# Kernel optimization log

Measured on AMD Instinct MI355X. Metric: run time of the kernel, lower is better.

The kernel has to match this reference:

```python
import jax, jax.numpy as jnp
import numpy as np

# Mistral-7B layer-0 config
D, DKV, DFF, NH, NKV, HD, BLK, VOCAB = 4096, 1024, 14336, 32, 8, 128, 64, 32000
THETA = 10000.0
NF4_CODE = jnp.array([-1.0, -0.6961928009986877, -0.5250730514526367, -0.39491748809814453,
                      -0.28444138169288635, -0.18477343022823334, -0.09105003625154495, 0.0,
                      0.07958029955625534, 0.16093020141124725, 0.24611230194568634,
                      0.33791524171829224, 0.44070982933044434, 0.5626170039176941,
                      0.7229568362236023, 1.0], dtype=jnp.float32)


def dequant_nf4(idx, absmax):
    # idx: int [out,in] 4-bit codes; absmax: [numel/BLK] blockwise scales
    w = jnp.take(NF4_CODE, idx.reshape(-1, BLK)) * absmax[:, None]
    return w.reshape(idx.shape)


def rmsnorm(x, w, eps=1e-5):
    return x * jax.lax.rsqrt(jnp.mean(x * x, axis=-1, keepdims=True) + eps) * w


def rope(x, pos):
    # x: [B,S,H,HD] -- HF rotate-half convention
    half = HD // 2
    inv = 1.0 / (THETA ** (jnp.arange(0, half, dtype=jnp.float32) / half))
    f = pos[:, None] * inv[None, :]                      # [S, half]
    cos = jnp.concatenate([jnp.cos(f), jnp.cos(f)], -1)[None, :, None, :]
    sin = jnp.concatenate([jnp.sin(f), jnp.sin(f)], -1)[None, :, None, :]
    x1, x2 = x[..., :half], x[..., half:]
    rot = jnp.concatenate([-x2, x1], -1)
    return x * cos + rot * sin


def setup_inputs() -> dict:
    key = jax.random.key(0)
    ks = jax.random.split(key, 20)
    B, S = 4, 512
    inp = {}
    inp["input_ids"] = jax.random.randint(ks[0], (B, S), 0, VOCAB, dtype=jnp.int32)
    inp["attention_mask"] = jnp.ones((B, S), dtype=jnp.int32)
    inp["embed_table"] = jax.random.normal(ks[1], (VOCAB, D), dtype=jnp.float32) * 0.02
    shapes = {"q": (D, D), "k": (DKV, D), "v": (DKV, D), "o": (D, D),
              "gate": (DFF, D), "up": (DFF, D), "down": (D, DFF)}
    for i, (n, sh) in enumerate(shapes.items()):
        inp["idx_" + n] = jax.random.randint(ks[2 + i], sh, 0, 16, dtype=jnp.int32)
        inp["absmax_" + n] = jax.random.uniform(ks[9 + i], (sh[0] * sh[1] // BLK,), dtype=jnp.float32) * 0.02
    inp["rms1_w"] = jnp.ones((D,), jnp.float32)
    inp["rms2_w"] = jnp.ones((D,), jnp.float32)
    inp["dp_w"] = jax.random.normal(ks[16], (50, D), jnp.float32) * 0.02
    inp["dp_b"] = jnp.zeros((50,), jnp.float32)
    return inp


def reference(input_ids, attention_mask, embed_table,
              idx_q, idx_k, idx_v, idx_o, idx_gate, idx_up, idx_down,
              absmax_q, absmax_k, absmax_v, absmax_o, absmax_gate, absmax_up, absmax_down,
              rms1_w, rms2_w, dp_w, dp_b):
    B, S = input_ids.shape
    h = embed_table[input_ids]                            # [B,S,D]

    # --- Mistral decoder layer 0 (hidden_states[1]) ---
    r = rmsnorm(h, rms1_w)
    Wq = dequant_nf4(idx_q, absmax_q)
    Wk = dequant_nf4(idx_k, absmax_k)
    Wv = dequant_nf4(idx_v, absmax_v)
    Wo = dequant_nf4(idx_o, absmax_o)
    q = (r @ Wq.T).reshape(B, S, NH, HD)
    k = (r @ Wk.T).reshape(B, S, NKV, HD)
    v = (r @ Wv.T).reshape(B, S, NKV, HD)
    pos = jnp.arange(S, dtype=jnp.float32)
    q, k = rope(q, pos), rope(k, pos)
    rep = NH // NKV
    k = jnp.repeat(k, rep, axis=2)
    v = jnp.repeat(v, rep, axis=2)
    scores = jnp.einsum('bqhd,bkhd->bhqk', q, k) / np.float32(np.sqrt(HD))
    causal = jnp.tril(jnp.ones((S, S), bool))
    m = causal[None, None] & (attention_mask[:, None, None, :] > 0)
    scores = jnp.where(m, scores, jnp.float32(-1e9))
    p = jax.nn.softmax(scores, axis=-1)
    ao = jnp.einsum('bhqk,bkhd->bqhd', p, v).reshape(B, S, D)
    h = h + ao @ Wo.T

    r2 = rmsnorm(h, rms2_w)
    Wg = dequant_nf4(idx_gate, absmax_gate)
    Wu = dequant_nf4(idx_up, absmax_up)
    Wd = dequant_nf4(idx_down, absmax_down)
    h = h + (jax.nn.silu(r2 @ Wg.T) * (r2 @ Wu.T)) @ Wd.T

    # --- last_token_pool + L2 normalize ---
    last = jnp.sum(attention_mask, axis=-1) - 1           # [B]
    pooled = h[jnp.arange(B), last]                       # [B,D]
    pooled = pooled / jnp.maximum(jnp.linalg.norm(pooled, axis=1, keepdims=True), 1e-12)

    # --- down_projection + query*entity node embeddings ---
    emb = pooled @ dp_w.T + dp_b                          # [B,50]
    bs = B // 2
    node = emb[:bs] * emb[bs:]                            # [bs,50]
    return node
```

## Files before the change

### kernel.cpp

```cpp
#include <hip/hip_runtime.h>
#include <stdint.h>
#include <math.h>

#define TOK 2048
#define DMODEL 4096
#define DFF 14336
#define SEQ 512

typedef float f32x4 __attribute__((ext_vector_type(4)));
typedef short s16x8 __attribute__((ext_vector_type(8)));
typedef unsigned short u16x8 __attribute__((ext_vector_type(8)));

__constant__ float NF4_TAB[16] = {
  -1.0f, -0.6961928009986877f, -0.5250730514526367f, -0.39491748809814453f,
  -0.28444138169288635f, -0.18477343022823334f, -0.09105003625154495f, 0.0f,
  0.07958029955625534f, 0.16093020141124725f, 0.24611230194568634f,
  0.33791524171829224f, 0.44070982933044434f, 0.5626170039176941f,
  0.7229568362236023f, 1.0f };

__device__ __forceinline__ uint16_t f2bf(float f) {
  union { float f; uint32_t u; } x; x.f = f;
  uint32_t r = (x.u + 0x7FFFu + ((x.u >> 16) & 1u)) >> 16;
  return (uint16_t)r;
}
__device__ __forceinline__ float bf2f(uint16_t u) {
  union { uint32_t u; float f; } x; x.u = ((uint32_t)u) << 16;
  return x.f;
}
__device__ __forceinline__ f32x4 mfma16(s16x8 a, s16x8 b, f32x4 c) {
  return __builtin_amdgcn_mfma_f32_16x16x32_bf16(a, b, c, 0, 0, 0);
}
__device__ __forceinline__ void gload_lds16(const void* g, void* l) {
  __builtin_amdgcn_global_load_lds(
    (const __attribute__((address_space(1))) unsigned int*)g,
    (__attribute__((address_space(3))) unsigned int*)l, 16, 0, 0);
}

__global__ __launch_bounds__(256) void k_last(const int* __restrict__ maskp,
                                              int* __restrict__ lastb)
{
  int wv = threadIdx.x >> 6, l = threadIdx.x & 63;
  int cnt = 0;
  for (int j = l; j < SEQ; j += 64) cnt += (maskp[wv * SEQ + j] > 0);
  #pragma unroll
  for (int off = 1; off < 64; off <<= 1) cnt += __shfl_xor(cnt, off);
  if (l == 0) lastb[wv] = cnt - 1;
}

__global__ __launch_bounds__(256) void k_dequant(const int* __restrict__ idx,
    const float* __restrict__ am, uint16_t* __restrict__ out, int nelems, int K)
{
  __shared__ float code[16];
  if (threadIdx.x < 16) code[threadIdx.x] = NF4_TAB[threadIdx.x];
  __syncthreads();
  int nch = nelems >> 3;
  int stride = gridDim.x * 256;
  for (int c = blockIdx.x * 256 + threadIdx.x; c < nch; c += stride) {
    int e = c << 3;
    int row = e / K;
    int kc = e - row * K;
    float a = am[c >> 3];
    int4 i0 = *(const int4*)(idx + e);
    int4 i1 = *(const int4*)(idx + e + 4);
    u16x8 pk;
    pk[0] = f2bf(code[i0.x] * a);
    pk[1] = f2bf(code[i0.y] * a);
    pk[2] = f2bf(code[i0.z] * a);
    pk[3] = f2bf(code[i0.w] * a);
    pk[4] = f2bf(code[i1.x] * a);
    pk[5] = f2bf(code[i1.y] * a);
    pk[6] = f2bf(code[i1.z] * a);
    pk[7] = f2bf(code[i1.w] * a);
    int dk = (kc & ~63) | (((((kc >> 3) & 7) ^ (row & 7))) << 3);
    *(u16x8*)(out + (size_t)row * K + dk) = pk;
  }
}

__global__ __launch_bounds__(256) void k_rms(const int* __restrict__ ids,
    const float* __restrict__ table, const float* __restrict__ w,
    uint16_t* __restrict__ r)
{
  int t = blockIdx.x, tid = threadIdx.x;
  int wv = tid >> 6, l = tid & 63;
  const float* src = table + (size_t)ids[t] * DMODEL;
  int d0 = tid * 16;
  float vals[16];
  float ss = 0.f;
  #pragma unroll
  for (int i = 0; i < 4; ++i) {
    float4 v4 = *(const float4*)(src + d0 + i * 4);
    vals[i*4+0] = v4.x; vals[i*4+1] = v4.y; vals[i*4+2] = v4.z; vals[i*4+3] = v4.w;
    ss += v4.x*v4.x + v4.y*v4.y + v4.z*v4.z + v4.w*v4.w;
  }
  #pragma unroll
  for (int off = 1; off < 64; off <<= 1) ss += __shfl_xor(ss, off);
  __shared__ float red[4];
  if (l == 0) red[wv] = ss;
  __syncthreads();
  float rs = rsqrtf((red[0]+red[1]+red[2]+red[3]) * (1.f/DMODEL) + 1e-5f);
  #pragma unroll
  for (int cth = 0; cth < 2; ++cth) {
    int dd = d0 + cth * 8;
    u16x8 pk;
    #pragma unroll
    for (int j = 0; j < 8; ++j) pk[j] = f2bf(vals[cth*8+j] * rs * w[dd + j]);
    int dsw = (dd & ~63) | (((((dd >> 3) & 7) ^ (t & 7))) << 3);
    *(u16x8*)(r + (size_t)t * DMODEL + dsw) = pk;
  }
}

__global__ __launch_bounds__(512, 2) void k_gemmkv(
    const uint16_t* __restrict__ A, const uint16_t* __restrict__ W,
    float* __restrict__ pout)
{
  constexpr int K = 4096;
  constexpr int NT = 16;
  __shared__ __align__(1024) uint16_t As_[2 * 256 * 64];
  __shared__ __align__(1024) uint16_t Bs_[2 * 256 * 64];
  const int tid = threadIdx.x;
  const int wid = tid >> 6, l = tid & 63;
  const int wr = wid >> 2, wc = wid & 3;
  const int n0 = blockIdx.x * 256, m0 = blockIdx.y * 256;
  const size_t kbase = blockIdx.z * 1024;
  const int lrow = l >> 3, lcb = (l & 7) * 16;

  auto stA = [&](int t, int h) {
    int ta = (t < NT) ? t : (t - NT);
    const char* g = (const char*)A +
        ((size_t)(m0 + h * 128 + wid * 16 + lrow) * K + kbase + ta * 64) * 2 + lcb;
    char* s = (char*)As_ + (t & 1) * 32768 + h * 16384 + wid * 2048;
    gload_lds16(g, s);
    gload_lds16(g + (size_t)8 * K * 2, s + 1024);
  };
  auto stB = [&](int t, int h) {
    int ta = (t < NT) ? t : (t - NT);
    const char* g = (const char*)W +
        ((size_t)(n0 + h * 128 + wid * 16 + lrow) * K + kbase + ta * 64) * 2 + lcb;
    char* s = (char*)Bs_ + (t & 1) * 32768 + h * 16384 + wid * 2048;
    gload_lds16(g, s);
    gload_lds16(g + (size_t)8 * K * 2, s + 1024);
  };

  const int cb0 = (((l >> 4) << 4)) ^ ((l & 7) << 4);
  const int cb1 = (64 + ((l >> 4) << 4)) ^ ((l & 7) << 4);

  const f32x4 Z4 = {0.f, 0.f, 0.f, 0.f};
  f32x4 acc[8][4];
  #pragma unroll
  for (int i = 0; i < 8; ++i)
    #pragma unroll
    for (int j = 0; j < 4; ++j) acc[i][j] = Z4;
  s16x8 bfr[4][2];

#define VMW asm volatile("s_waitcnt vmcnt(6)" ::: "memory")
#define PHASE(DB, Q, READB, STG) {                                          \
    const char* abase = (const char*)As_ + (DB) * 32768;                    \
    s16x8 af[2][2];                                                         \
    _Pragma("unroll") for (int mm = 0; mm < 2; ++mm) {                      \
      int arow = ((2 * (2 * (Q) + mm) + wr) * 16 + (l & 15)) * 128;         \
      af[mm][0] = *(const s16x8*)(abase + arow + cb0);                      \
      af[mm][1] = *(const s16x8*)(abase + arow + cb1);                      \
    }                                                                       \
    if (READB) {                                                            \
      const char* bbase = (const char*)Bs_ + (DB) * 32768;                  \
      _Pragma("unroll") for (int nn = 0; nn < 4; ++nn) {                    \
        int brow = (wc * 64 + nn * 16 + (l & 15)) * 128;                    \
        bfr[nn][0] = *(const s16x8*)(bbase + brow + cb0);                   \
        bfr[nn][1] = *(const s16x8*)(bbase + brow + cb1);                   \
      }                                                                     \
    }                                                                       \
    STG;                                                                    \
    __builtin_amdgcn_s_barrier();                                           \
    asm volatile("s_waitcnt lgkmcnt(0)" ::: "memory");                      \
    __builtin_amdgcn_sched_barrier(0);                                      \
    __builtin_amdgcn_s_setprio(1);                                          \
    _Pragma("unroll") for (int mm = 0; mm < 2; ++mm)                        \
      _Pragma("unroll") for (int nn = 0; nn < 4; ++nn) {                    \
        acc[2 * (Q) + mm][nn] = mfma16(af[mm][0], bfr[nn][0], acc[2 * (Q) + mm][nn]); \
        acc[2 * (Q) + mm][nn] = mfma16(af[mm][1], bfr[nn][1], acc[2 * (Q) + mm][nn]); \
      }                                                                     \
    __builtin_amdgcn_s_setprio(0);                                          \
    __builtin_amdgcn_s_barrier();                                           \
  }

  stB(0, 0); stA(0, 0); stB(0, 1); stA(0, 1);
  stB(1, 0); stA(1, 0); stB(1, 1);
  VMW;
  __builtin_amdgcn_s_barrier();

  for (int it = 0; it < NT / 2; ++it) {
    int t0 = 2 * it, t1 = t0 + 1;
    PHASE(0, 0, 1, stA(t1, 1));
    PHASE(0, 1, 0, stB(t0 + 2, 0));
    PHASE(0, 2, 0, stA(t0 + 2, 0));
    PHASE(0, 3, 0, { stB(t0 + 2, 1); VMW; });
    PHASE(1, 0, 1, stA(t0 + 2, 1));
    PHASE(1, 1, 0, stB(t1 + 2, 0));
    PHASE(1, 2, 0, stA(t1 + 2, 0));
    PHASE(1, 3, 0, { stB(t1 + 2, 1); VMW; });
  }
  asm volatile("s_waitcnt vmcnt(0)" ::: "memory");
  __builtin_amdgcn_s_barrier();
#undef PHASE
#undef VMW

  float* po = pout + (size_t)blockIdx.z * 2048 * 2048;
  #pragma unroll
  for (int mf = 0; mf < 8; ++mf)
    #pragma unroll
    for (int nf = 0; nf < 4; ++nf)
      #pragma unroll
      for (int r = 0; r < 4; ++r) {
        int row = m0 + (2 * mf + wr) * 16 + ((l >> 4) << 2) + r;
        int col = n0 + wc * 64 + nf * 16 + (l & 15);
        po[(size_t)row * 2048 + col] = acc[mf][nf][r];
      }
}

__global__ __launch_bounds__(256) void k_redrope(const float* __restrict__ p,
    uint16_t* __restrict__ kv)
{
  int t = blockIdx.x, tid = threadIdx.x;
  const size_t zs = (size_t)2048 * 2048;
  auto sum4 = [&](int c) -> float {
    size_t o = (size_t)t * 2048 + c;
    return p[o] + p[o + zs] + p[o + 2 * zs] + p[o + 3 * zs];
  };
  float pos = (float)(t & (SEQ - 1));
  for (int pi = tid; pi < 512; pi += 256) {
    int hh = pi >> 6, j = pi & 63;
    int c1 = hh * 128 + j, c2 = c1 + 64;
    float s1 = sum4(c1), s2 = sum4(c2);
    float f = pos * expf(-(float)j * 0.14391156831212787f);
    float sn, cs;
    sincosf(f, &sn, &cs);
    kv[(size_t)t * 2048 + c1] = f2bf(s1 * cs - s2 * sn);
    kv[(size_t)t * 2048 + c2] = f2bf(s2 * cs + s1 * sn);
  }
  for (int c = 1024 + tid; c < 2048; c += 256)
    kv[(size_t)t * 2048 + c] = f2bf(sum4(c));
}

__global__ __launch_bounds__(256) void k_prep_r4(const uint16_t* __restrict__ rbuf,
    const int* __restrict__ lastb, float* __restrict__ r4f)
{
  int r = blockIdx.x;
  int t = r * SEQ + lastb[r];
  const uint16_t* src = rbuf + (size_t)t * DMODEL;
  for (int k = threadIdx.x * 8; k < DMODEL; k += 2048) {
    int so = (k & ~63) | (((((k >> 3) & 7) ^ (t & 7))) << 3);
    u16x8 v = *(const u16x8*)(src + so);
    #pragma unroll
    for (int j = 0; j < 8; ++j) r4f[r * DMODEL + k + j] = bf2f(v[j]);
  }
}

template<int MODE>
__global__ __launch_bounds__(256) void k_gemv4(const int* __restrict__ idx,
    const float* __restrict__ am, const float* __restrict__ a4,
    float* __restrict__ out, const float* __restrict__ table,
    const int* __restrict__ ids, const int* __restrict__ lastb)
{
  __shared__ float As[4 * 4096];
  __shared__ float code[16];
  if (threadIdx.x < 16) code[threadIdx.x] = NF4_TAB[threadIdx.x];
  for (int i = threadIdx.x * 4; i < 4 * 4096; i += 1024)
    *(float4*)(As + i) = *(const float4*)(a4 + i);
  __syncthreads();
  int wv = threadIdx.x >> 6, l = threadIdx.x & 63;
  int lhi = l >> 4;
  for (int n = blockIdx.x * 4 + wv; n < 4096; n += gridDim.x * 4) {
    const int4* ip = (const int4*)(idx + (size_t)n * 4096);
    const float* ap = am + (size_t)n * 64;
    float a0 = 0.f, a1 = 0.f, a2 = 0.f, a3 = 0.f;
    #pragma unroll
    for (int kk = 0; kk < 16; ++kk) {
      int4 iv = ip[kk * 64 + l];
      float sc = ap[kk * 4 + lhi];
      float w0 = code[iv.x] * sc, w1 = code[iv.y] * sc;
      float w2 = code[iv.z] * sc, w3 = code[iv.w] * sc;
      const float* A0 = As + kk * 256 + l * 4;
      f32x4 v0 = *(const f32x4*)A0;
      f32x4 v1 = *(const f32x4*)(A0 + 4096);
      f32x4 v2 = *(const f32x4*)(A0 + 8192);
      f32x4 v3 = *(const f32x4*)(A0 + 12288);
      a0 = fmaf(w0, v0[0], fmaf(w1, v0[1], fmaf(w2, v0[2], fmaf(w3, v0[3], a0))));
      a1 = fmaf(w0, v1[0], fmaf(w1, v1[1], fmaf(w2, v1[2], fmaf(w3, v1[3], a1))));
      a2 = fmaf(w0, v2[0], fmaf(w1, v2[1], fmaf(w2, v2[2], fmaf(w3, v2[3], a2))));
      a3 = fmaf(w0, v3[0], fmaf(w1, v3[1], fmaf(w2, v3[2], fmaf(w3, v3[3], a3))));
    }
    #pragma unroll
    for (int off = 1; off < 64; off <<= 1) {
      a0 += __shfl_xor(a0, off); a1 += __shfl_xor(a1, off);
      a2 += __shfl_xor(a2, off); a3 += __shfl_xor(a3, off);
    }
    if (l == 0) {
      float av[4] = {a0, a1, a2, a3};
      #pragma unroll
      for (int r = 0; r < 4; ++r) {
        float base = 0.f;
        if (MODE == 1)
          base = table[(size_t)ids[r * SEQ + lastb[r]] * DMODEL + n];
        out[r * 4096 + n] = base + av[r];
      }
    }
  }
}

__global__ __launch_bounds__(256) void k_gemv_gu(const int* __restrict__ idxg,
    const float* __restrict__ amg, const int* __restrict__ idxu,
    const float* __restrict__ amu, const float* __restrict__ a4,
    uint16_t* __restrict__ hm)
{
  __shared__ float As[4 * 4096];
  __shared__ float code[16];
  if (threadIdx.x < 16) code[threadIdx.x] = NF4_TAB[threadIdx.x];
  for (int i = threadIdx.x * 4; i < 4 * 4096; i += 1024)
    *(float4*)(As + i) = *(const float4*)(a4 + i);
  __syncthreads();
  int wv = threadIdx.x >> 6, l = threadIdx.x & 63;
  int lhi = l >> 4;
  for (int n = blockIdx.x * 4 + wv; n < DFF; n += gridDim.x * 4) {
    const int4* ipg = (const int4*)(idxg + (size_t)n * 4096);
    const int4* ipu = (const int4*)(idxu + (size_t)n * 4096);
    const float* apg = amg + (size_t)n * 64;
    const float* apu = amu + (size_t)n * 64;
    float g0 = 0.f, g1 = 0.f, g2 = 0.f, g3 = 0.f;
    float u0 = 0.f, u1 = 0.f, u2 = 0.f, u3 = 0.f;
    #pragma unroll 8
    for (int kk = 0; kk < 16; ++kk) {
      int4 ig = ipg[kk * 64 + l];
      int4 iu = ipu[kk * 64 + l];
      float sg = apg[kk * 4 + lhi];
      float su = apu[kk * 4 + lhi];
      float wg0 = code[ig.x] * sg, wg1 = code[ig.y] * sg;
      float wg2 = code[ig.z] * sg, wg3 = code[ig.w] * sg;
      float wu0 = code[iu.x] * su, wu1 = code[iu.y] * su;
      float wu2 = code[iu.z] * su, wu3 = code[iu.w] * su;
      const float* A0 = As + kk * 256 + l * 4;
      f32x4 v0 = *(const f32x4*)A0;
      f32x4 v1 = *(const f32x4*)(A0 + 4096);
      f32x4 v2 = *(const f32x4*)(A0 + 8192);
      f32x4 v3 = *(const f32x4*)(A0 + 12288);
      g0 = fmaf(wg0, v0[0], fmaf(wg1, v0[1], fmaf(wg2, v0[2], fmaf(wg3, v0[3], g0))));
      g1 = fmaf(wg0, v1[0], fmaf(wg1, v1[1], fmaf(wg2, v1[2], fmaf(wg3, v1[3], g1))));
      g2 = fmaf(wg0, v2[0], fmaf(wg1, v2[1], fmaf(wg2, v2[2], fmaf(wg3, v2[3], g2))));
      g3 = fmaf(wg0, v3[0], fmaf(wg1, v3[1], fmaf(wg2, v3[2], fmaf(wg3, v3[3], g3))));
      u0 = fmaf(wu0, v0[0], fmaf(wu1, v0[1], fmaf(wu2, v0[2], fmaf(wu3, v0[3], u0))));
      u1 = fmaf(wu0, v1[0], fmaf(wu1, v1[1], fmaf(wu2, v1[2], fmaf(wu3, v1[3], u1))));
      u2 = fmaf(wu0, v2[0], fmaf(wu1, v2[1], fmaf(wu2, v2[2], fmaf(wu3, v2[3], u2))));
      u3 = fmaf(wu0, v3[0], fmaf(wu1, v3[1], fmaf(wu2, v3[2], fmaf(wu3, v3[3], u3))));
    }
    #pragma unroll
    for (int off = 1; off < 64; off <<= 1) {
      g0 += __shfl_xor(g0, off); g1 += __shfl_xor(g1, off);
      g2 += __shfl_xor(g2, off); g3 += __shfl_xor(g3, off);
      u0 += __shfl_xor(u0, off); u1 += __shfl_xor(u1, off);
      u2 += __shfl_xor(u2, off); u3 += __shfl_xor(u3, off);
    }
    if (l == 0) {
      float gv[4] = {g0, g1, g2, g3};
      float uv[4] = {u0, u1, u2, u3};
      #pragma unroll
      for (int r = 0; r < 4; ++r) {
        float g = gv[r];
        hm[(size_t)r * DFF + n] = f2bf((g / (1.f + __expf(-g))) * uv[r]);
      }
    }
  }
}

__global__ __launch_bounds__(256) void k_gemv_down(const int* __restrict__ idx,
    const float* __restrict__ am, const uint16_t* __restrict__ hm,
    const float* __restrict__ h4, float* __restrict__ h4f)
{
  __shared__ uint16_t As[4 * 14336];
  __shared__ float code[16];
  if (threadIdx.x < 16) code[threadIdx.x] = NF4_TAB[threadIdx.x];
  for (int i = threadIdx.x * 8; i < 4 * 14336; i += 2048)
    *(u16x8*)(As + i) = *(const u16x8*)(hm + i);
  __syncthreads();
  int wv = threadIdx.x >> 6, l = threadIdx.x & 63;
  int lhi = l >> 4;
  for (int n = blockIdx.x * 4 + wv; n < 4096; n += gridDim.x * 4) {
    const int4* ip = (const int4*)(idx + (size_t)n * 14336);
    const float* ap = am + (size_t)n * 224;
    float a0 = 0.f, a1 = 0.f, a2 = 0.f, a3 = 0.f;
    #pragma unroll 8
    for (int kk = 0; kk < 56; ++kk) {
      int4 iv = ip[kk * 64 + l];
      float sc = ap[kk * 4 + lhi];
      float w0 = code[iv.x] * sc, w1 = code[iv.y] * sc;
      float w2 = code[iv.z] * sc, w3 = code[iv.w] * sc;
      int k0 = kk * 256 + l * 4;
      const uint16_t* B0 = As + k0;
      #pragma unroll
      for (int r = 0; r < 4; ++r) {
        u16x8 hv8;
        *(uint2*)&hv8 = *(const uint2*)(B0 + r * 14336);
        float x0 = bf2f(hv8[0]), x1 = bf2f(hv8[1]);
        float x2 = bf2f(hv8[2]), x3 = bf2f(hv8[3]);
        float t = fmaf(w0, x0, fmaf(w1, x1, fmaf(w2, x2, w3 * x3)));
        if (r == 0) a0 += t; else if (r == 1) a1 += t;
        else if (r == 2) a2 += t; else a3 += t;
      }
    }
    #pragma unroll
    for (int off = 1; off < 64; off <<= 1) {
      a0 += __shfl_xor(a0, off); a1 += __shfl_xor(a1, off);
      a2 += __shfl_xor(a2, off); a3 += __shfl_xor(a3, off);
    }
    if (l == 0) {
      float av[4] = {a0, a1, a2, a3};
      #pragma unroll
      for (int r = 0; r < 4; ++r)
        h4f[r * 4096 + n] = h4[r * 4096 + n] + av[r];
    }
  }
}

__global__ __launch_bounds__(256) void k_attn4(const float* __restrict__ q4,
    const uint16_t* __restrict__ kv, const int* __restrict__ maskp,
    const int* __restrict__ lastb, float* __restrict__ ao4)
{
  int hh = blockIdx.x, b = blockIdx.y;
  int kvh = hh >> 2;
  int tid = threadIdx.x;
  __shared__ float qs[128];
  __shared__ float sarr[512];
  __shared__ float red[256];
  __shared__ float oacc[2][128];
  int last = lastb[b];
  if (tid < 128) {
    int d = tid, j = d & 63;
    float f = (float)last * expf(-(float)j * 0.14391156831212787f);
    float sn, cs;
    sincosf(f, &sn, &cs);
    const float* q = q4 + b * 4096 + hh * 128;
    float v = (d < 64) ? (q[d] * cs - q[d + 64] * sn)
                       : (q[d] * cs + q[d - 64] * sn);
    qs[d] = v * 0.08838834764831845f;
  }
  __syncthreads();
  float sl[2];
  #pragma unroll
  for (int h2 = 0; h2 < 2; ++h2) {
    int jj = tid + h2 * 256;
    bool valid = (jj <= last) && (maskp[b * SEQ + jj] > 0);
    float s = -1e9f;
    if (valid) {
      s = 0.f;
      const uint16_t* kp = kv + ((size_t)(b * SEQ + jj)) * 2048 + kvh * 128;
      #pragma unroll
      for (int c = 0; c < 16; ++c) {
        u16x8 kvv = *(const u16x8*)(kp + c * 8);
        #pragma unroll
        for (int e = 0; e < 8; ++e)
          s = fmaf(qs[c * 8 + e], bf2f(kvv[e]), s);
      }
    }
    sarr[jj] = s;
    sl[h2] = s;
  }
  red[tid] = fmaxf(sl[0], sl[1]);
  __syncthreads();
  for (int s = 128; s > 0; s >>= 1) {
    if (tid < s) red[tid] = fmaxf(red[tid], red[tid + s]);
    __syncthreads();
  }
  float m = red[0];
  __syncthreads();
  float ps = 0.f;
  #pragma unroll
  for (int h2 = 0; h2 < 2; ++h2) {
    int jj = tid + h2 * 256;
    float pe = __expf(sarr[jj] - m);
    ps += pe;
    sarr[jj] = pe;
  }
  red[tid] = ps;
  __syncthreads();
  for (int s = 128; s > 0; s >>= 1) {
    if (tid < s) red[tid] += red[tid + s];
    __syncthreads();
  }
  float inv = 1.f / red[0];
  __syncthreads();
  int half = tid >> 7, d = tid & 127;
  float acc = 0.f;
  const uint16_t* vp = kv + ((size_t)(b * SEQ + half * 256)) * 2048 + 1024 + kvh * 128 + d;
  for (int j = 0; j < 256; ++j)
    acc = fmaf(sarr[half * 256 + j], bf2f(vp[(size_t)j * 2048]), acc);
  oacc[half][d] = acc;
  __syncthreads();
  if (tid < 128)
    ao4[b * 4096 + hh * 128 + tid] = (oacc[0][tid] + oacc[1][tid]) * inv;
}

__global__ __launch_bounds__(256) void k_rms2(const float* __restrict__ h4,
    const float* __restrict__ w, float* __restrict__ r2f)
{
  int b = blockIdx.x, tid = threadIdx.x;
  int wv = tid >> 6, l = tid & 63;
  int d0 = tid * 16;
  const float* src = h4 + b * 4096;
  float vals[16];
  float ss = 0.f;
  #pragma unroll
  for (int i = 0; i < 4; ++i) {
    float4 v4 = *(const float4*)(src + d0 + i * 4);
    vals[i*4+0] = v4.x; vals[i*4+1] = v4.y; vals[i*4+2] = v4.z; vals[i*4+3] = v4.w;
    ss += v4.x*v4.x + v4.y*v4.y + v4.z*v4.z + v4.w*v4.w;
  }
  #pragma unroll
  for (int off = 1; off < 64; off <<= 1) ss += __shfl_xor(ss, off);
  __shared__ float red[4];
  if (l == 0) red[wv] = ss;
  __syncthreads();
  float rs = rsqrtf((red[0]+red[1]+red[2]+red[3]) * (1.f/4096.f) + 1e-5f);
  #pragma unroll
  for (int i = 0; i < 16; ++i)
    r2f[b * 4096 + d0 + i] = vals[i] * rs * w[d0 + i];
}

__global__ __launch_bounds__(256) void k_pool3(const float* __restrict__ h4f,
    const float* __restrict__ dpw, const float* __restrict__ dpb,
    float* __restrict__ out)
{
  int o = blockIdx.x;
  int tid = threadIdx.x, wv = tid >> 6, l = tid & 63;
  __shared__ float dsh[4], nsh[4];
  const float* row = h4f + wv * 4096;
  const float* wrow = dpw + (size_t)o * 4096;
  float d1 = 0.f, ss = 0.f;
  for (int d = l * 4; d < 4096; d += 256) {
    float4 v = *(const float4*)(row + d);
    float4 u = *(const float4*)(wrow + d);
    d1 += v.x*u.x + v.y*u.y + v.z*u.z + v.w*u.w;
    ss += v.x*v.x + v.y*v.y + v.z*v.z + v.w*v.w;
  }
  #pragma unroll
  for (int off = 1; off < 64; off <<= 1) {
    d1 += __shfl_xor(d1, off);
    ss += __shfl_xor(ss, off);
  }
  if (l == 0) { dsh[wv] = d1; nsh[wv] = fmaxf(sqrtf(ss), 1e-12f); }
  __syncthreads();
  if (tid < 2) {
    float b = dpb[o];
    float e1 = dsh[tid] / nsh[tid] + b;
    float e2 = dsh[tid + 2] / nsh[tid + 2] + b;
    out[tid * 50 + o] = e1 * e2;
  }
}

extern "C" void kernel_launch(void* const* d_in, const int* in_sizes, int n_in,
                              void* d_out, int out_size, void* d_ws, size_t ws_size,
                              hipStream_t stream) {
  const int*   ids   = (const int*)d_in[0];
  const int*   maskp = (const int*)d_in[1];
  const float* table = (const float*)d_in[2];
  const int* idxp[7];
  const float* amp[7];
  if (in_sizes[4] == in_sizes[3] / 64) {
    for (int i = 0; i < 7; ++i) {
      idxp[i] = (const int*)d_in[3 + 2 * i];
      amp[i]  = (const float*)d_in[4 + 2 * i];
    }
  } else {
    for (int i = 0; i < 7; ++i) {
      idxp[i] = (const int*)d_in[3 + i];
      amp[i]  = (const float*)d_in[10 + i];
    }
  }
  const float* rms1 = (const float*)d_in[17];
  const float* rms2w = (const float*)d_in[18];
  const float* dpw  = (const float*)d_in[19];
  const float* dpb  = (const float*)d_in[20];
  float* out = (float*)d_out;

  char* p = (char*)d_ws;
  int*      lastb = (int*)p;      p += 256;
  float*    r4f   = (float*)p;    p += 4 * 4096 * 4;
  float*    q4    = (float*)p;    p += 4 * 4096 * 4;
  float*    ao4   = (float*)p;    p += 4 * 4096 * 4;
  float*    h4    = (float*)p;    p += 4 * 4096 * 4;
  float*    r2f   = (float*)p;    p += 4 * 4096 * 4;
  float*    h4f   = (float*)p;    p += 4 * 4096 * 4;
  uint16_t* hm4   = (uint16_t*)p; p += 4 * DFF * 2 + 512;
  uint16_t* kvbuf = (uint16_t*)p; p += (size_t)TOK * 2048 * 2;
  uint16_t* rbuf  = (uint16_t*)p; p += (size_t)TOK * DMODEL * 2;
  uint16_t* wbuf  = (uint16_t*)p; p += (size_t)2048 * DMODEL * 2;
  float*    pbuf  = (float*)p;    p += (size_t)4 * 2048 * 2048 * 4;

  k_last<<<1, 256, 0, stream>>>(maskp, lastb);
  k_rms<<<TOK, 256, 0, stream>>>(ids, table, rms1, rbuf);

  k_dequant<<<2048, 256, 0, stream>>>(idxp[1], amp[1], wbuf, 1024 * DMODEL, DMODEL);
  k_dequant<<<2048, 256, 0, stream>>>(idxp[2], amp[2], wbuf + (size_t)1024 * DMODEL, 1024 * DMODEL, DMODEL);
  k_gemmkv<<<dim3(8, 8, 4), 512, 0, stream>>>(rbuf, wbuf, pbuf);
  k_redrope<<<TOK, 256, 0, stream>>>(pbuf, kvbuf);

  k_prep_r4<<<4, 256, 0, stream>>>(rbuf, lastb, r4f);
  k_gemv4<0><<<512, 256, 0, stream>>>(idxp[0], amp[0], r4f, q4, nullptr, nullptr, nullptr);

  k_attn4<<<dim3(32, 4), 256, 0, stream>>>(q4, kvbuf, maskp, lastb, ao4);

  k_gemv4<1><<<512, 256, 0, stream>>>(idxp[3], amp[3], ao4, h4, table, ids, lastb);

  k_rms2<<<4, 256, 0, stream>>>(h4, rms2w, r2f);
  k_gemv_gu<<<448, 256, 0, stream>>>(idxp[4], amp[4], idxp[5], amp[5], r2f, hm4);
  k_gemv_down<<<256, 256, 0, stream>>>(idxp[6], amp[6], hm4, h4, h4f);

  k_pool3<<<50, 256, 0, stream>>>(h4f, dpw, dpb, out);
}
```

Baseline: 411.8 us.

## Interleave 4-row activations and drop LDS staging in NF4 GEMV kernels

Activation vectors for the four pooled rows are stored interleaved ([k][4]) so each GEMV reads them straight from global/L2 as one float4 per k instead of copying the full activation into LDS per block. The grids grow to one output row per wave (no grid-stride loops), and the gate/up intermediate stays in fp32 rather than bf16. The aim is to remove the per-block LDS fill (up to 112KB for the down projection), which capped occupancy and repeated global reads. The cost is more L2 traffic for activations and a single-block RMSNorm kernel.

```diff
diff --git a/kernel.cpp b/kernel.cpp
--- a/kernel.cpp
+++ b/kernel.cpp
@@ -242,7 +242,7 @@
 }
 
 __global__ __launch_bounds__(256) void k_prep_r4(const uint16_t* __restrict__ rbuf,
-    const int* __restrict__ lastb, float* __restrict__ r4f)
+    const int* __restrict__ lastb, float* __restrict__ r4i)
 {
   int r = blockIdx.x;
   int t = r * SEQ + lastb[r];
@@ -251,177 +251,162 @@
     int so = (k & ~63) | (((((k >> 3) & 7) ^ (t & 7))) << 3);
     u16x8 v = *(const u16x8*)(src + so);
     #pragma unroll
-    for (int j = 0; j < 8; ++j) r4f[r * DMODEL + k + j] = bf2f(v[j]);
+    for (int j = 0; j < 8; ++j) r4i[(k + j) * 4 + r] = bf2f(v[j]);
   }
 }
 
 template<int MODE>
-__global__ __launch_bounds__(256) void k_gemv4(const int* __restrict__ idx,
-    const float* __restrict__ am, const float* __restrict__ a4,
-    float* __restrict__ out, const float* __restrict__ table,
+__global__ __launch_bounds__(256) void k_gemv4i(const int* __restrict__ idx,
+    const float* __restrict__ am, const float* __restrict__ a4i,
+    float* __restrict__ out4i, const float* __restrict__ table,
     const int* __restrict__ ids, const int* __restrict__ lastb)
 {
-  __shared__ float As[4 * 4096];
   __shared__ float code[16];
   if (threadIdx.x < 16) code[threadIdx.x] = NF4_TAB[threadIdx.x];
-  for (int i = threadIdx.x * 4; i < 4 * 4096; i += 1024)
-    *(float4*)(As + i) = *(const float4*)(a4 + i);
   __syncthreads();
   int wv = threadIdx.x >> 6, l = threadIdx.x & 63;
   int lhi = l >> 4;
-  for (int n = blockIdx.x * 4 + wv; n < 4096; n += gridDim.x * 4) {
-    const int4* ip = (const int4*)(idx + (size_t)n * 4096);
-    const float* ap = am + (size_t)n * 64;
-    float a0 = 0.f, a1 = 0.f, a2 = 0.f, a3 = 0.f;
-    #pragma unroll
-    for (int kk = 0; kk < 16; ++kk) {
-      int4 iv = ip[kk * 64 + l];
-      float sc = ap[kk * 4 + lhi];
-      float w0 = code[iv.x] * sc, w1 = code[iv.y] * sc;
-      float w2 = code[iv.z] * sc, w3 = code[iv.w] * sc;
-      const float* A0 = As + kk * 256 + l * 4;
-      f32x4 v0 = *(const f32x4*)A0;
-      f32x4 v1 = *(const f32x4*)(A0 + 4096);
-      f32x4 v2 = *(const f32x4*)(A0 + 8192);
-      f32x4 v3 = *(const f32x4*)(A0 + 12288);
-      a0 = fmaf(w0, v0[0], fmaf(w1, v0[1], fmaf(w2, v0[2], fmaf(w3, v0[3], a0))));
-      a1 = fmaf(w0, v1[0], fmaf(w1, v1[1], fmaf(w2, v1[2], fmaf(w3, v1[3], a1))));
-      a2 = fmaf(w0, v2[0], fmaf(w1, v2[1], fmaf(w2, v2[2], fmaf(w3, v2[3], a2))));
-      a3 = fmaf(w0, v3[0], fmaf(w1, v3[1], fmaf(w2, v3[2], fmaf(w3, v3[3], a3))));
+  int n = blockIdx.x * 4 + wv;
+  const int4* ip = (const int4*)(idx + (size_t)n * 4096);
+  const float* ap = am + (size_t)n * 64;
+  float a0 = 0.f, a1 = 0.f, a2 = 0.f, a3 = 0.f;
+  #pragma unroll
+  for (int kk = 0; kk < 16; ++kk) {
+    int4 iv = ip[kk * 64 + l];
+    float sc = ap[kk * 4 + lhi];
+    float w0 = code[iv.x] * sc, w1 = code[iv.y] * sc;
+    float w2 = code[iv.z] * sc, w3 = code[iv.w] * sc;
+    const float* A0 = a4i + (kk * 256 + l * 4) * 4;
+    f32x4 k0 = *(const f32x4*)(A0);
+    f32x4 k1 = *(const f32x4*)(A0 + 4);
+    f32x4 k2 = *(const f32x4*)(A0 + 8);
+    f32x4 k3 = *(const f32x4*)(A0 + 12);
+    a0 = fmaf(w0, k0[0], fmaf(w1, k1[0], fmaf(w2, k2[0], fmaf(w3, k3[0], a0))));
+    a1 = fmaf(w0, k0[1], fmaf(w1, k1[1], fmaf(w2, k2[1], fmaf(w3, k3[1], a1))));
+    a2 = fmaf(w0, k0[2], fmaf(w1, k1[2], fmaf(w2, k2[2], fmaf(w3, k3[2], a2))));
+    a3 = fmaf(w0, k0[3], fmaf(w1, k1[3], fmaf(w2, k2[3], fmaf(w3, k3[3], a3))));
+  }
+  #pragma unroll
+  for (int off = 1; off < 64; off <<= 1) {
+    a0 += __shfl_xor(a0, off); a1 += __shfl_xor(a1, off);
+    a2 += __shfl_xor(a2, off); a3 += __shfl_xor(a3, off);
+  }
+  if (l == 0) {
+    f32x4 o;
+    o[0] = a0; o[1] = a1; o[2] = a2; o[3] = a3;
+    if (MODE == 1) {
+      #pragma unroll
+      for (int r = 0; r < 4; ++r)
+        o[r] += table[(size_t)ids[r * SEQ + lastb[r]] * DMODEL + n];
     }
-    #pragma unroll
-    for (int off = 1; off < 64; off <<= 1) {
-      a0 += __shfl_xor(a0, off); a1 += __shfl_xor(a1, off);
-      a2 += __shfl_xor(a2, off); a3 += __shfl_xor(a3, off);
-    }
-    if (l == 0) {
-      float av[4] = {a0, a1, a2, a3};
-      #pragma unroll
-      for (int r = 0; r < 4; ++r) {
-        float base = 0.f;
-        if (MODE == 1)
-          base = table[(size_t)ids[r * SEQ + lastb[r]] * DMODEL + n];
-        out[r * 4096 + n] = base + av[r];
-      }
-    }
+    *(f32x4*)(out4i + (size_t)n * 4) = o;
   }
 }
 
 __global__ __launch_bounds__(256) void k_gemv_gu(const int* __restrict__ idxg,
     const float* __restrict__ amg, const int* __restrict__ idxu,
-    const float* __restrict__ amu, const float* __restrict__ a4,
-    uint16_t* __restrict__ hm)
-{
-  __shared__ float As[4 * 4096];
+    const float* __restrict__ amu, const float* __restrict__ a4i,
+    float* __restrict__ hm4i)
+{
   __shared__ float code[16];
   if (threadIdx.x < 16) code[threadIdx.x] = NF4_TAB[threadIdx.x];
-  for (int i = threadIdx.x * 4; i < 4 * 4096; i += 1024)
-    *(float4*)(As + i) = *(const float4*)(a4 + i);
   __syncthreads();
   int wv = threadIdx.x >> 6, l = threadIdx.x & 63;
   int lhi = l >> 4;
-  for (int n = blockIdx.x * 4 + wv; n < DFF; n += gridDim.x * 4) {
-    const int4* ipg = (const int4*)(idxg + (size_t)n * 4096);
-    const int4* ipu = (const int4*)(idxu + (size_t)n * 4096);
-    const float* apg = amg + (size_t)n * 64;
-    const float* apu = amu + (size_t)n * 64;
-    float g0 = 0.f, g1 = 0.f, g2 = 0.f, g3 = 0.f;
-    float u0 = 0.f, u1 = 0.f, u2 = 0.f, u3 = 0.f;
-    #pragma unroll 8
-    for (int kk = 0; kk < 16; ++kk) {
-      int4 ig = ipg[kk * 64 + l];
-      int4 iu = ipu[kk * 64 + l];
-      float sg = apg[kk * 4 + lhi];
-      float su = apu[kk * 4 + lhi];
-      float wg0 = code[ig.x] * sg, wg1 = code[ig.y] * sg;
-      float wg2 = code[ig.z] * sg, wg3 = code[ig.w] * sg;
-      float wu0 = code[iu.x] * su, wu1 = code[iu.y] * su;
-      float wu2 = code[iu.z] * su, wu3 = code[iu.w] * su;
-      const float* A0 = As + kk * 256 + l * 4;
-      f32x4 v0 = *(const f32x4*)A0;
-      f32x4 v1 = *(const f32x4*)(A0 + 4096);
-      f32x4 v2 = *(const f32x4*)(A0 + 8192);
-      f32x4 v3 = *(const f32x4*)(A0 + 12288);
-      g0 = fmaf(wg0, v0[0], fmaf(wg1, v0[1], fmaf(wg2, v0[2], fmaf(wg3, v0[3], g0))));
-      g1 = fmaf(wg0, v1[0], fmaf(wg1, v1[1], fmaf(wg2, v1[2], fmaf(wg3, v1[3], g1))));
-      g2 = fmaf(wg0, v2[0], fmaf(wg1, v2[1], fmaf(wg2, v2[2], fmaf(wg3, v2[3], g2))));
-      g3 = fmaf(wg0, v3[0], fmaf(wg1, v3[1], fmaf(wg2, v3[2], fmaf(wg3, v3[3], g3))));
-      u0 = fmaf(wu0, v0[0], fmaf(wu1, v0[1], fmaf(wu2, v0[2], fmaf(wu3, v0[3], u0))));
-      u1 = fmaf(wu0, v1[0], fmaf(wu1, v1[1], fmaf(wu2, v1[2], fmaf(wu3, v1[3], u1))));
-      u2 = fmaf(wu0, v2[0], fmaf(wu1, v2[1], fmaf(wu2, v2[2], fmaf(wu3, v2[3], u2))));
-      u3 = fmaf(wu0, v3[0], fmaf(wu1, v3[1], fmaf(wu2, v3[2], fmaf(wu3, v3[3], u3))));
-    }
-    #pragma unroll
-    for (int off = 1; off < 64; off <<= 1) {
-      g0 += __shfl_xor(g0, off); g1 += __shfl_xor(g1, off);
-      g2 += __shfl_xor(g2, off); g3 += __shfl_xor(g3, off);
-      u0 += __shfl_xor(u0, off); u1 += __shfl_xor(u1, off);
-      u2 += __shfl_xor(u2, off); u3 += __shfl_xor(u3, off);
-    }
-    if (l == 0) {
-      float gv[4] = {g0, g1, g2, g3};
-      float uv[4] = {u0, u1, u2, u3};
-      #pragma unroll
-      for (int r = 0; r < 4; ++r) {
-        float g = gv[r];
-        hm[(size_t)r * DFF + n] = f2bf((g / (1.f + __expf(-g))) * uv[r]);
-      }
-    }
+  int n = blockIdx.x * 4 + wv;
+  const int4* ipg = (const int4*)(idxg + (size_t)n * 4096);
+  const int4* ipu = (const int4*)(idxu + (size_t)n * 4096);
+  const float* apg = amg + (size_t)n * 64;
+  const float* apu = amu + (size_t)n * 64;
+  float g0 = 0.f, g1 = 0.f, g2 = 0.f, g3 = 0.f;
+  float u0 = 0.f, u1 = 0.f, u2 = 0.f, u3 = 0.f;
+  #pragma unroll
+  for (int kk = 0; kk < 16; ++kk) {
+    int4 ig = ipg[kk * 64 + l];
+    int4 iu = ipu[kk * 64 + l];
+    float sg = apg[kk * 4 + lhi];
+    float su = apu[kk * 4 + lhi];
+    float wg0 = code[ig.x] * sg, wg1 = code[ig.y] * sg;
+    float wg2 = code[ig.z] * sg, wg3 = code[ig.w] * sg;
+    float wu0 = code[iu.x] * su, wu1 = code[iu.y] * su;
+    float wu2 = code[iu.z] * su, wu3 = code[iu.w] * su;
+    const float* A0 = a4i + (kk * 256 + l * 4) * 4;
+    f32x4 k0 = *(const f32x4*)(A0);
+    f32x4 k1 = *(const f32x4*)(A0 + 4);
+    f32x4 k2 = *(const f32x4*)(A0 + 8);
+    f32x4 k3 = *(const f32x4*)(A0 + 12);
+    g0 = fmaf(wg0, k0[0], fmaf(wg1, k1[0], fmaf(wg2, k2[0], fmaf(wg3, k3[0], g0))));
+    g1 = fmaf(wg0, k0[1], fmaf(wg1, k1[1], fmaf(wg2, k2[1], fmaf(wg3, k3[1], g1))));
+    g2 = fmaf(wg0, k0[2], fmaf(wg1, k1[2], fmaf(wg2, k2[2], fmaf(wg3, k3[2], g2))));
+    g3 = fmaf(wg0, k0[3], fmaf(wg1, k1[3], fmaf(wg2, k2[3], fmaf(wg3, k3[3], g3))));
+    u0 = fmaf(wu0, k0[0], fmaf(wu1, k1[0], fmaf(wu2, k2[0], fmaf(wu3, k3[0], u0))));
+    u1 = fmaf(wu0, k0[1], fmaf(wu1, k1[1], fmaf(wu2, k2[1], fmaf(wu3, k3[1], u1))));
+    u2 = fmaf(wu0, k0[2], fmaf(wu1, k1[2], fmaf(wu2, k2[2], fmaf(wu3, k3[2], u2))));
+    u3 = fmaf(wu0, k0[3], fmaf(wu1, k1[3], fmaf(wu2, k2[3], fmaf(wu3, k3[3], u3))));
+  }
+  #pragma unroll
+  for (int off = 1; off < 64; off <<= 1) {
+    g0 += __shfl_xor(g0, off); g1 += __shfl_xor(g1, off);
+    g2 += __shfl_xor(g2, off); g3 += __shfl_xor(g3, off);
+    u0 += __shfl_xor(u0, off); u1 += __shfl_xor(u1, off);
+    u2 += __shfl_xor(u2, off); u3 += __shfl_xor(u3, off);
+  }
+  if (l == 0) {
+    f32x4 o;
+    o[0] = (g0 / (1.f + __expf(-g0))) * u0;
+    o[1] = (g1 / (1.f + __expf(-g1))) * u1;
+    o[2] = (g2 / (1.f + __expf(-g2))) * u2;
+    o[3] = (g3 / (1.f + __expf(-g3))) * u3;
+    *(f32x4*)(hm4i + (size_t)n * 4) = o;
   }
 }
 
 __global__ __launch_bounds__(256) void k_gemv_down(const int* __restrict__ idx,
-    const float* __restrict__ am, const uint16_t* __restrict__ hm,
-    const float* __restrict__ h4, float* __restrict__ h4f)
-{
-  __shared__ uint16_t As[4 * 14336];
+    const float* __restrict__ am, const float* __restrict__ hm4i,
+    const float* __restrict__ h4i, float* __restrict__ h4r)
+{
   __shared__ float code[16];
   if (threadIdx.x < 16) code[threadIdx.x] = NF4_TAB[threadIdx.x];
-  for (int i = threadIdx.x * 8; i < 4 * 14336; i += 2048)
-    *(u16x8*)(As + i) = *(const u16x8*)(hm + i);
   __syncthreads();
   int wv = threadIdx.x >> 6, l = threadIdx.x & 63;
   int lhi = l >> 4;
-  for (int n = blockIdx.x * 4 + wv; n < 4096; n += gridDim.x * 4) {
-    const int4* ip = (const int4*)(idx + (size_t)n * 14336);
-    const float* ap = am + (size_t)n * 224;
-    float a0 = 0.f, a1 = 0.f, a2 = 0.f, a3 = 0.f;
-    #pragma unroll 8
-    for (int kk = 0; kk < 56; ++kk) {
-      int4 iv = ip[kk * 64 + l];
-      float sc = ap[kk * 4 + lhi];
-      float w0 = code[iv.x] * sc, w1 = code[iv.y] * sc;
-      float w2 = code[iv.z] * sc, w3 = code[iv.w] * sc;
-      int k0 = kk * 256 + l * 4;
-      const uint16_t* B0 = As + k0;
-      #pragma unroll
-      for (int r = 0; r < 4; ++r) {
-        u16x8 hv8;
-        *(uint2*)&hv8 = *(const uint2*)(B0 + r * 14336);
-        float x0 = bf2f(hv8[0]), x1 = bf2f(hv8[1]);
-        float x2 = bf2f(hv8[2]), x3 = bf2f(hv8[3]);
-        float t = fmaf(w0, x0, fmaf(w1, x1, fmaf(w2, x2, w3 * x3)));
-        if (r == 0) a0 += t; else if (r == 1) a1 += t;
-        else if (r == 2) a2 += t; else a3 += t;
-      }
-    }
-    #pragma unroll
-    for (int off = 1; off < 64; off <<= 1) {
-      a0 += __shfl_xor(a0, off); a1 += __shfl_xor(a1, off);
-      a2 += __shfl_xor(a2, off); a3 += __shfl_xor(a3, off);
-    }
-    if (l == 0) {
-      float av[4] = {a0, a1, a2, a3};
-      #pragma unroll
-      for (int r = 0; r < 4; ++r)
-        h4f[r * 4096 + n] = h4[r * 4096 + n] + av[r];
-    }
-  }
-}
-
-__global__ __launch_bounds__(256) void k_attn4(const float* __restrict__ q4,
+  int n = blockIdx.x * 4 + wv;
+  const int4* ip = (const int4*)(idx + (size_t)n * 14336);
+  const float* ap = am + (size_t)n * 224;
+  float a0 = 0.f, a1 = 0.f, a2 = 0.f, a3 = 0.f;
+  #pragma unroll 8
+  for (int kk = 0; kk < 56; ++kk) {
+    int4 iv = ip[kk * 64 + l];
+    float sc = ap[kk * 4 + lhi];
+    float w0 = code[iv.x] * sc, w1 = code[iv.y] * sc;
+    float w2 = code[iv.z] * sc, w3 = code[iv.w] * sc;
+    const float* A0 = hm4i + (kk * 256 + l * 4) * 4;
+    f32x4 k0 = *(const f32x4*)(A0);
+    f32x4 k1 = *(const f32x4*)(A0 + 4);
+    f32x4 k2 = *(const f32x4*)(A0 + 8);
+    f32x4 k3 = *(const f32x4*)(A0 + 12);
+    a0 = fmaf(w0, k0[0], fmaf(w1, k1[0], fmaf(w2, k2[0], fmaf(w3, k3[0], a0))));
+    a1 = fmaf(w0, k0[1], fmaf(w1, k1[1], fmaf(w2, k2[1], fmaf(w3, k3[1], a1))));
+    a2 = fmaf(w0, k0[2], fmaf(w1, k1[2], fmaf(w2, k2[2], fmaf(w3, k3[2], a2))));
+    a3 = fmaf(w0, k0[3], fmaf(w1, k1[3], fmaf(w2, k2[3], fmaf(w3, k3[3], a3))));
+  }
+  #pragma unroll
+  for (int off = 1; off < 64; off <<= 1) {
+    a0 += __shfl_xor(a0, off); a1 += __shfl_xor(a1, off);
+    a2 += __shfl_xor(a2, off); a3 += __shfl_xor(a3, off);
+  }
+  if (l == 0) {
+    f32x4 hr = *(const f32x4*)(h4i + (size_t)n * 4);
+    h4r[0 * 4096 + n] = hr[0] + a0;
+    h4r[1 * 4096 + n] = hr[1] + a1;
+    h4r[2 * 4096 + n] = hr[2] + a2;
+    h4r[3 * 4096 + n] = hr[3] + a3;
+  }
+}
+
+__global__ __launch_bounds__(256) void k_attn4(const float* __restrict__ q4i,
     const uint16_t* __restrict__ kv, const int* __restrict__ maskp,
-    const int* __restrict__ lastb, float* __restrict__ ao4)
+    const int* __restrict__ lastb, float* __restrict__ ao4i)
 {
   int hh = blockIdx.x, b = blockIdx.y;
   int kvh = hh >> 2;
@@ -436,9 +421,10 @@
     float f = (float)last * expf(-(float)j * 0.14391156831212787f);
     float sn, cs;
     sincosf(f, &sn, &cs);
-    const float* q = q4 + b * 4096 + hh * 128;
-    float v = (d < 64) ? (q[d] * cs - q[d + 64] * sn)
-                       : (q[d] * cs + q[d - 64] * sn);
+    float qd  = q4i[(hh * 128 + d) * 4 + b];
+    float qd2 = (d < 64) ? q4i[(hh * 128 + d + 64) * 4 + b]
+                         : q4i[(hh * 128 + d - 64) * 4 + b];
+    float v = (d < 64) ? (qd * cs - qd2 * sn) : (qd * cs + qd2 * sn);
     qs[d] = v * 0.08838834764831845f;
   }
   __syncthreads();
@@ -494,43 +480,50 @@
   oacc[half][d] = acc;
   __syncthreads();
   if (tid < 128)
-    ao4[b * 4096 + hh * 128 + tid] = (oacc[0][tid] + oacc[1][tid]) * inv;
-}
-
-__global__ __launch_bounds__(256) void k_rms2(const float* __restrict__ h4,
-    const float* __restrict__ w, float* __restrict__ r2f)
-{
-  int b = blockIdx.x, tid = threadIdx.x;
-  int wv = tid >> 6, l = tid & 63;
-  int d0 = tid * 16;
-  const float* src = h4 + b * 4096;
-  float vals[16];
-  float ss = 0.f;
-  #pragma unroll
-  for (int i = 0; i < 4; ++i) {
-    float4 v4 = *(const float4*)(src + d0 + i * 4);
-    vals[i*4+0] = v4.x; vals[i*4+1] = v4.y; vals[i*4+2] = v4.z; vals[i*4+3] = v4.w;
-    ss += v4.x*v4.x + v4.y*v4.y + v4.z*v4.z + v4.w*v4.w;
-  }
-  #pragma unroll
-  for (int off = 1; off < 64; off <<= 1) ss += __shfl_xor(ss, off);
-  __shared__ float red[4];
+    ao4i[(hh * 128 + tid) * 4 + b] = (oacc[0][tid] + oacc[1][tid]) * inv;
+}
+
+__global__ __launch_bounds__(256) void k_rms2i(const float* __restrict__ h4i,
+    const float* __restrict__ w, float* __restrict__ r2i)
+{
+  int tid = threadIdx.x, wv = tid >> 6, l = tid & 63;
+  f32x4 vals[16];
+  f32x4 ss = {0.f, 0.f, 0.f, 0.f};
+  #pragma unroll
+  for (int i = 0; i < 16; ++i) {
+    vals[i] = *(const f32x4*)(h4i + (size_t)(tid + i * 256) * 4);
+    ss += vals[i] * vals[i];
+  }
+  #pragma unroll
+  for (int off = 1; off < 64; off <<= 1) {
+    ss[0] += __shfl_xor(ss[0], off);
+    ss[1] += __shfl_xor(ss[1], off);
+    ss[2] += __shfl_xor(ss[2], off);
+    ss[3] += __shfl_xor(ss[3], off);
+  }
+  __shared__ f32x4 red[4];
   if (l == 0) red[wv] = ss;
   __syncthreads();
-  float rs = rsqrtf((red[0]+red[1]+red[2]+red[3]) * (1.f/4096.f) + 1e-5f);
-  #pragma unroll
-  for (int i = 0; i < 16; ++i)
-    r2f[b * 4096 + d0 + i] = vals[i] * rs * w[d0 + i];
-}
-
-__global__ __launch_bounds__(256) void k_pool3(const float* __restrict__ h4f,
+  f32x4 tot = red[0] + red[1] + red[2] + red[3];
+  f32x4 rs;
+  #pragma unroll
+  for (int r = 0; r < 4; ++r) rs[r] = rsqrtf(tot[r] * (1.f / 4096.f) + 1e-5f);
+  #pragma unroll
+  for (int i = 0; i < 16; ++i) {
+    float wk = w[tid + i * 256];
+    f32x4 o = vals[i] * rs * wk;
+    *(f32x4*)(r2i + (size_t)(tid + i * 256) * 4) = o;
+  }
+}
+
+__global__ __launch_bounds__(256) void k_pool3(const float* __restrict__ h4r,
     const float* __restrict__ dpw, const float* __restrict__ dpb,
     float* __restrict__ out)
 {
   int o = blockIdx.x;
   int tid = threadIdx.x, wv = tid >> 6, l = tid & 63;
   __shared__ float dsh[4], nsh[4];
-  const float* row = h4f + wv * 4096;
+  const float* row = h4r + wv * 4096;
   const float* wrow = dpw + (size_t)o * 4096;
   float d1 = 0.f, ss = 0.f;
   for (int d = l * 4; d < 4096; d += 256) {
@@ -581,13 +574,13 @@
 
   char* p = (char*)d_ws;
   int*      lastb = (int*)p;      p += 256;
-  float*    r4f   = (float*)p;    p += 4 * 4096 * 4;
-  float*    q4    = (float*)p;    p += 4 * 4096 * 4;
-  float*    ao4   = (float*)p;    p += 4 * 4096 * 4;
-  float*    h4    = (float*)p;    p += 4 * 4096 * 4;
-  float*    r2f   = (float*)p;    p += 4 * 4096 * 4;
-  float*    h4f   = (float*)p;    p += 4 * 4096 * 4;
-  uint16_t* hm4   = (uint16_t*)p; p += 4 * DFF * 2 + 512;
+  float*    r4i   = (float*)p;    p += 4 * 4096 * 4;
+  float*    q4i   = (float*)p;    p += 4 * 4096 * 4;
+  float*    ao4i  = (float*)p;    p += 4 * 4096 * 4;
+  float*    h4i   = (float*)p;    p += 4 * 4096 * 4;
+  float*    r2i   = (float*)p;    p += 4 * 4096 * 4;
+  float*    h4r   = (float*)p;    p += 4 * 4096 * 4;
+  float*    hm4i  = (float*)p;    p += (size_t)4 * DFF * 4 + 512;
   uint16_t* kvbuf = (uint16_t*)p; p += (size_t)TOK * 2048 * 2;
   uint16_t* rbuf  = (uint16_t*)p; p += (size_t)TOK * DMODEL * 2;
   uint16_t* wbuf  = (uint16_t*)p; p += (size_t)2048 * DMODEL * 2;
@@ -601,16 +594,16 @@
   k_gemmkv<<<dim3(8, 8, 4), 512, 0, stream>>>(rbuf, wbuf, pbuf);
   k_redrope<<<TOK, 256, 0, stream>>>(pbuf, kvbuf);
 
-  k_prep_r4<<<4, 256, 0, stream>>>(rbuf, lastb, r4f);
-  k_gemv4<0><<<512, 256, 0, stream>>>(idxp[0], amp[0], r4f, q4, nullptr, nullptr, nullptr);
-
-  k_attn4<<<dim3(32, 4), 256, 0, stream>>>(q4, kvbuf, maskp, lastb, ao4);
-
-  k_gemv4<1><<<512, 256, 0, stream>>>(idxp[3], amp[3], ao4, h4, table, ids, lastb);
-
-  k_rms2<<<4, 256, 0, stream>>>(h4, rms2w, r2f);
-  k_gemv_gu<<<448, 256, 0, stream>>>(idxp[4], amp[4], idxp[5], amp[5], r2f, hm4);
-  k_gemv_down<<<256, 256, 0, stream>>>(idxp[6], amp[6], hm4, h4, h4f);
-
-  k_pool3<<<50, 256, 0, stream>>>(h4f, dpw, dpb, out);
-}
+  k_prep_r4<<<4, 256, 0, stream>>>(rbuf, lastb, r4i);
+  k_gemv4i<0><<<1024, 256, 0, stream>>>(idxp[0], amp[0], r4i, q4i, nullptr, nullptr, nullptr);
+
+  k_attn4<<<dim3(32, 4), 256, 0, stream>>>(q4i, kvbuf, maskp, lastb, ao4i);
+
+  k_gemv4i<1><<<1024, 256, 0, stream>>>(idxp[3], amp[3], ao4i, h4i, table, ids, lastb);
+
+  k_rms2i<<<1, 256, 0, stream>>>(h4i, rms2w, r2i);
+  k_gemv_gu<<<3584, 256, 0, stream>>>(idxp[4], amp[4], idxp[5], amp[5], r2i, hm4i);
+  k_gemv_down<<<1024, 256, 0, stream>>>(idxp[6], amp[6], hm4i, h4i, h4r);
+
+  k_pool3<<<50, 256, 0, stream>>>(h4r, dpw, dpb, out);
+}
```

Result: no change. 415.6 us (+0.9%).
